# Kernel optimization log

Measured on AMD Instinct MI355X. Metric: run time of the kernel, lower is better.

## Reference

```python
import jax, jax.numpy as jnp
import numpy as np
from jax import lax

DILATIONS = (1, 2, 4)
K = 3        # kernel_size
HORIZON = 6


def _gcn(x, src, dst, W, b, n):
    # PyG GCNConv with self-loops: D^{-1/2}(A+I)D^{-1/2} X W + b
    xw = x @ W                                                # [N,H]
    e = src.shape[0]
    deg = 1.0 + jax.ops.segment_sum(jnp.ones((e,), x.dtype), dst, num_segments=n)
    dinv = lax.rsqrt(deg)                                     # [N]
    msg = xw[src] * (dinv[src] * dinv[dst])[:, None]          # [E,H]
    agg = jax.ops.segment_sum(msg, dst, num_segments=n)       # [N,H]
    return agg + xw * (dinv * dinv)[:, None] + b


def _cell(x, src, dst, win, gcn_w, gcn_b, conv_w, conv_b, proj_w, proj_b):
    n = x.shape[0]
    hg = jax.nn.relu(_gcn(x, src, dst, gcn_w, gcn_b, n))      # [N,H]
    tcn_in = jnp.concatenate([win[:, 1:], hg[:, None]], axis=1)  # [N,K,H]
    hin = jnp.transpose(tcn_in, (0, 2, 1))                    # [N,H,K]
    outs = []
    for i, d in enumerate(DILATIONS):
        p = (K - 1) * d // 2
        y = lax.conv_general_dilated(hin, conv_w[i], (1,), [(p, p)],
                                     rhs_dilation=(d,),
                                     dimension_numbers=('NCH', 'OIH', 'NCH'))
        outs.append(y[:, :, -1] + conv_b[i])                  # last temporal position, [N,H]
    h_new = jnp.concatenate(outs, axis=1) @ proj_w.T + proj_b  # [N,H]
    new_win = jnp.concatenate([win[:, 1:], h_new[:, None]], axis=1)
    return h_new, new_win


def reference(x_seq, edge_index_seq, edge_attr_seq, mask_seq, id_seq,
              gcn_w, gcn_b, conv_w, conv_b, proj_w, proj_b, head_w, head_b):
    T, N, _ = x_seq.shape
    H = gcn_w.shape[1]
    win0 = jnp.zeros((N, K, H), x_seq.dtype)

    def enc_step(win, inp):
        x_t, ei_t = inp
        _, win = _cell(x_t, ei_t[0], ei_t[1], win,
                       gcn_w, gcn_b, conv_w, conv_b, proj_w, proj_b)
        return win, None

    win, _ = lax.scan(enc_step, win0, (x_seq, edge_index_seq))

    src, dst = edge_index_seq[-1, 0], edge_index_seq[-1, 1]

    def dec_step(carry, _):
        win, inp = carry
        h_new, win = _cell(inp, src, dst, win,
                           gcn_w, gcn_b, conv_w, conv_b, proj_w, proj_b)
        y = h_new @ head_w.T + head_b                          # [N,C]
        return (win, y), y

    _, preds = lax.scan(dec_step, (win, x_seq[-1]), None, length=HORIZON)
    return preds  # [horizon, N, out_channels]


def setup_inputs() -> dict:
    T, N, F, E, H, C = 12, 20000, 16, 320000, 128, 16
    key = jax.random.key(0)
    ks = jax.random.split(key, 12)
    return {
        'x_seq': jax.random.normal(ks[0], (T, N, F), jnp.float32),
        'edge_index_seq': jax.random.randint(ks[1], (T, 2, E), 0, N, jnp.int64),
        'edge_attr_seq': jax.random.normal(ks[2], (T, E, 1), jnp.float32),
        'mask_seq': jnp.ones((T, N), jnp.bool_),
        'id_seq': jnp.tile(jnp.arange(N, dtype=jnp.int32)[None], (T, 1)),
        'gcn_w': jax.random.normal(ks[3], (F, H), jnp.float32) * 0.1,
        'gcn_b': jnp.zeros((H,), jnp.float32),
        'conv_w': jax.random.normal(ks[4], (3, H, H, K), jnp.float32) * 0.05,
        'conv_b': jnp.zeros((3, H), jnp.float32),
        'proj_w': jax.random.normal(ks[5], (H, 3 * H), jnp.float32) * 0.05,
        'proj_b': jnp.zeros((H,), jnp.float32),
        'head_w': jax.random.normal(ks[6], (C, H), jnp.float32) * 0.05,
        'head_b': jnp.zeros((C,), jnp.float32),
    }
```

## Files before the change

### kernel.cpp

```cpp
#include <hip/hip_runtime.h>

#define NN 20000
#define NP 20032
#define EE 320000
#define TT 12
#define HH 128
#define FF 16
#define CC 16
#define HOR 6

#define NB 313
#define WPT 84
#define CHE 3812

#define AGG_GRID 1896
#define HGA_GRID 15024

typedef __attribute__((ext_vector_type(8))) short short8;
typedef __attribute__((ext_vector_type(4))) float f32x4;

__device__ __forceinline__ float blo(unsigned int u) {
    union { float f; unsigned int i; } v; v.i = u << 16; return v.f;
}
__device__ __forceinline__ float bhi(unsigned int u) {
    union { float f; unsigned int i; } v; v.i = u & 0xffff0000u; return v.f;
}
__device__ __forceinline__ unsigned short f2b(float f) {
    union { float f; unsigned int i; } v; v.f = f;
    unsigned int x = v.i;
    return (unsigned short)((x + 0x7fffu + ((x >> 16) & 1u)) >> 16);
}
__device__ __forceinline__ unsigned int pck(float lo, float hi) {
    return ((unsigned int)f2b(hi) << 16) | f2b(lo);
}
__device__ __forceinline__ void addrow(float* acc, uint4 r) {
    acc[0] += blo(r.x); acc[1] += bhi(r.x);
    acc[2] += blo(r.y); acc[3] += bhi(r.y);
    acc[4] += blo(r.z); acc[5] += bhi(r.z);
    acc[6] += blo(r.w); acc[7] += bhi(r.w);
}

__global__ void k_zero(int* p, int n) {
    int i = blockIdx.x * 256 + threadIdx.x;
    if (i < n) p[i] = 0;
}

__global__ __launch_bounds__(512) void k_binA(const int* __restrict__ ei,
                                              int* __restrict__ gData,
                                              int* __restrict__ pcnt,
                                              int* __restrict__ pofs) {
    int wg = blockIdx.x;
    int t = wg / WPT, w = wg - t * WPT;
    __shared__ int lcnt[NB];
    __shared__ int sm[512];
    __shared__ __align__(16) int elist[CHE];
    int tid = threadIdx.x;
    for (int i = tid; i < NB; i += 512) lcnt[i] = 0;
    __syncthreads();
    int e0 = w * CHE, e1 = min(EE, e0 + CHE);
    int total = e1 - e0;
    const int* si = ei + (size_t)t * 2 * EE;
    const int* di = si + EE;
    int eA = e0 + tid * 4, eB = eA + 2048;
    bool hA = eA < e1, hB = eB < e1;
    int sA[4], dA[4], pA[4], sB[4], dB[4], pB[4];
    if (hA) {
        int4 s4 = *(const int4*)(si + eA);
        int4 d4 = *(const int4*)(di + eA);
        sA[0] = s4.x; sA[1] = s4.y; sA[2] = s4.z; sA[3] = s4.w;
        dA[0] = d4.x; dA[1] = d4.y; dA[2] = d4.z; dA[3] = d4.w;
    }
    if (hB) {
        int4 s4 = *(const int4*)(si + eB);
        int4 d4 = *(const int4*)(di + eB);
        sB[0] = s4.x; sB[1] = s4.y; sB[2] = s4.z; sB[3] = s4.w;
        dB[0] = d4.x; dB[1] = d4.y; dB[2] = d4.z; dB[3] = d4.w;
    }
    if (hA) {
#pragma unroll
        for (int k = 0; k < 4; k++) pA[k] = atomicAdd(&lcnt[dA[k] >> 6], 1);
    }
    if (hB) {
#pragma unroll
        for (int k = 0; k < 4; k++) pB[k] = atomicAdd(&lcnt[dB[k] >> 6], 1);
    }
    __syncthreads();
    sm[tid] = (tid < NB) ? lcnt[tid] : 0;
    __syncthreads();
    for (int off = 1; off < 512; off <<= 1) {
        int u = (tid >= off) ? sm[tid - off] : 0;
        __syncthreads();
        sm[tid] += u;
        __syncthreads();
    }
    if (tid < NB) {
        int v = lcnt[tid];
        int ex = sm[tid] - v;
        size_t o = (size_t)(t * WPT + w) * NB + tid;
        pcnt[o] = v;
        pofs[o] = ex;
        sm[tid] = ex;
    }
    __syncthreads();
    if (hA) {
#pragma unroll
        for (int k = 0; k < 4; k++) {
            int b = dA[k] >> 6;
            elist[sm[b] + pA[k]] = ((dA[k] & 63) << 16) | sA[k];
        }
    }
    if (hB) {
#pragma unroll
        for (int k = 0; k < 4; k++) {
            int b = dB[k] >> 6;
            elist[sm[b] + pB[k]] = ((dB[k] & 63) << 16) | sB[k];
        }
    }
    __syncthreads();
    int* gOut = gData + (size_t)(t * WPT + w) * CHE;
    for (int i = tid * 4; i < total; i += 2048)
        *(int4*)(gOut + i) = *(const int4*)&elist[i];
}

__global__ __launch_bounds__(512) void k_bscan2(const int* __restrict__ pcnt,
                                                int* __restrict__ bbase,
                                                int* __restrict__ rowptr) {
    int t = blockIdx.x, tid = threadIdx.x;
    __shared__ int sm[512];
    int v = 0;
    if (tid < NB)
        for (int w = 0; w < WPT; w++) v += pcnt[(size_t)(t * WPT + w) * NB + tid];
    sm[tid] = v;
    __syncthreads();
    for (int off = 1; off < 512; off <<= 1) {
        int u = (tid >= off) ? sm[tid - off] : 0;
        __syncthreads();
        sm[tid] += u;
        __syncthreads();
    }
    if (tid < NB) bbase[t * NB + tid] = sm[tid] - v;
    if (tid == 511) rowptr[(size_t)t * (NN + 1) + NN] = sm[511];
}

__global__ __launch_bounds__(256) void k_placeB(const int* __restrict__ gData,
                                                const int* __restrict__ pcnt,
                                                const int* __restrict__ pofs,
                                                const int* __restrict__ bbase,
                                                int* __restrict__ rowptr,
                                                float* __restrict__ dinv,
                                                unsigned short* __restrict__ csr) {
    int t = blockIdx.x / NB, b = blockIdx.x - t * NB;
    int tid = threadIdx.x;
    __shared__ int scnt[WPT], sofs[WPT], cofs[WPT + 1];
    __shared__ int elist[2048];
    __shared__ int cnt64[64], lofs[64], place[64];
    if (tid < WPT) {
        size_t o = (size_t)(t * WPT + tid) * NB + b;
        scnt[tid] = pcnt[o];
        sofs[tid] = pofs[o];
    }
    if (tid < 64) cnt64[tid] = 0;
    __syncthreads();
    if (tid == 0) {
        int s = 0;
        for (int w = 0; w < WPT; w++) { cofs[w] = s; s += scnt[w]; }
        cofs[WPT] = s;
    }
    __syncthreads();
    int total = cofs[WPT];
    int wv = tid >> 6, lane = tid & 63;
    for (int w = wv; w < WPT; w += 4) {
        int c = scnt[w], o = cofs[w];
        const int* sp = gData + (size_t)(t * WPT + w) * CHE + sofs[w];
        for (int i = lane; i < c; i += 64) elist[o + i] = sp[i];
    }
    __syncthreads();
    for (int i = tid; i < total; i += 256) atomicAdd(&cnt64[elist[i] >> 16], 1);
    __syncthreads();
    if (tid == 0) {
        int s = 0;
        for (int j = 0; j < 64; j++) { lofs[j] = s; place[j] = s; s += cnt64[j]; }
    }
    __syncthreads();
    int base = bbase[t * NB + b];
    int n = b * 64 + tid;
    if (tid < 64 && n < NN) {
        rowptr[(size_t)t * (NN + 1) + n] = base + lofs[tid];
        dinv[(size_t)t * NN + n] = rsqrtf(1.0f + (float)cnt64[tid]);
    }
    unsigned short* cbase = csr + (size_t)t * EE + base;
    for (int i = tid; i < total; i += 256) {
        int en = elist[i];
        int r = atomicAdd(&place[en >> 16], 1);
        cbase[r] = (unsigned short)(en & 0xffff);
    }
}

__global__ void k_count(const int* __restrict__ ei, int* __restrict__ cnt) {
    int idx = blockIdx.x * 256 + threadIdx.x;
    if (idx >= TT * EE) return;
    int t = idx / EE, e = idx - t * EE;
    int d = ei[t * 2 * EE + EE + e];
    atomicAdd(&cnt[t * NN + d], 1);
}

__global__ void k_dinvF(const int* __restrict__ cnt, float* __restrict__ dinv) {
    int idx = blockIdx.x * 256 + threadIdx.x;
    if (idx >= TT * NN) return;
    dinv[idx] = 1.0f / sqrtf(1.0f + (float)cnt[idx]);
}

__global__ void k_scan(const int* __restrict__ cnt, int* __restrict__ rowptr, int* __restrict__ wofs) {
    int t = blockIdx.x;
    const int* c = cnt + t * NN;
    int* rp = rowptr + t * (NN + 1);
    int* wo = wofs + t * NN;
    __shared__ int sums[1024];
    int tid = threadIdx.x;
    const int CH2 = 20;
    int base = tid * CH2;
    int loc[CH2];
    int s = 0;
    for (int i = 0; i < CH2; i++) { int ix = base + i; int v = (ix < NN) ? c[ix] : 0; loc[i] = s; s += v; }
    sums[tid] = s;
    __syncthreads();
    for (int off = 1; off < 1024; off <<= 1) {
        int v = (tid >= off) ? sums[tid - off] : 0;
        __syncthreads();
        sums[tid] += v;
        __syncthreads();
    }
    int excl = (tid > 0) ? sums[tid - 1] : 0;
    for (int i = 0; i < CH2; i++) {
        int ix = base + i;
        if (ix < NN) { int e = excl + loc[i]; rp[ix] = e; wo[ix] = e; }
    }
    if (tid == 1023) rp[NN] = sums[1023];
}

__global__ void k_place(const int* __restrict__ ei, int* __restrict__ wofs,
                        unsigned short* __restrict__ csr) {
    int idx = blockIdx.x * 256 + threadIdx.x;
    if (idx >= TT * EE) return;
    int t = idx / EE, e = idx - t * EE;
    int s = ei[t * 2 * EE + e];
    int d = ei[t * 2 * EE + EE + e];
    int pos = atomicAdd(&wofs[t * NN + d], 1);
    csr[t * EE + pos] = (unsigned short)s;
}

__global__ void k_wprepB(const float* __restrict__ cw, const float* __restrict__ pw,
                         const float* __restrict__ cb, const float* __restrict__ pb,
                         unsigned short* __restrict__ Bpk, float* __restrict__ Bf32,
                         float* __restrict__ bias) {
    int idx = blockIdx.x * 256 + threadIdx.x;
    if (blockIdx.x == 192) {
        int h = threadIdx.x;
        if (h < HH) {
            float m = pb[h];
            for (int d = 0; d < 3; d++)
                for (int o = 0; o < HH; o++)
                    m += cb[d * HH + o] * pw[h * 384 + d * HH + o];
            bias[h] = m;
        }
        return;
    }
    if (idx >= 384 * HH) return;
    int kk = idx / HH, h = idx - kk * HH;
    float m = 0.f;
    if (kk < 128) {
        int i = kk;
        for (int o = 0; o < HH; o++)
            m += cw[((1 * HH + o) * HH + i) * 3 + 0] * pw[h * 384 + 128 + o];
    } else if (kk < 256) {
        int i = kk - 128;
        for (int o = 0; o < HH; o++)
            m += cw[((0 * HH + o) * HH + i) * 3 + 0] * pw[h * 384 + o];
    } else {
        int i = kk - 256;
        for (int d = 0; d < 3; d++)
            for (int o = 0; o < HH; o++)
                m += cw[((d * HH + o) * HH + i) * 3 + 1] * pw[h * 384 + d * HH + o];
    }
    Bf32[kk * HH + h] = m;
    int ki = kk >> 5, r = kk & 31, q = r >> 3, j = r & 7, nt = h >> 4, ln = q * 16 + (h & 15);
    Bpk[(size_t)((ki * 8 + nt) * 64 + ln) * 8 + j] = f2b(m);
}

__global__ __launch_bounds__(128) void k_tchain(const float* __restrict__ Bf32,
                                                const float* __restrict__ biasT,
                                                unsigned short* __restrict__ Bq,
                                                float* __restrict__ biasQ) {
    __shared__ float v1[128], v2[128];
    int c = threadIdx.x;
    int r = blockIdx.x;
    const float* M2 = Bf32;
    const float* M1 = Bf32 + 128 * HH;
    const float* Mh = Bf32 + 256 * HH;
    if (r < 128) {
        int q4 = (r & 31) >> 3, jj = r & 7, rb = r >> 5;
        v1[c] = Mh[r * HH + c];
        v2[c] = 0.f;
        __syncthreads();
        {
            float val = v1[c];
            int kb0 = 10 * 4 + rb, nt0 = c >> 4, ln = q4 * 16 + (c & 15);
            Bq[((size_t)(kb0 * 16 + nt0) * 64 + ln) * 8 + jj] = f2b(val);
            int kb1 = 11 * 4 + rb, nt1 = 8 + (c >> 4);
            Bq[((size_t)(kb1 * 16 + nt1) * 64 + ln) * 8 + jj] = f2b(val);
        }
        for (int j = 1; j < 12; j++) {
            float acc = 0.f;
            for (int k = 0; k < 128; k++)
                acc += v1[k] * M1[k * HH + c] + v2[k] * M2[k * HH + c];
            __syncthreads();
            v2[c] = v1[c]; v1[c] = acc;
            __syncthreads();
            int ln = q4 * 16 + (c & 15);
            if (j <= 10) {
                int kb = (10 - j) * 4 + rb, nt = c >> 4;
                Bq[((size_t)(kb * 16 + nt) * 64 + ln) * 8 + jj] = f2b(acc);
            }
            {
                int kb = (11 - j) * 4 + rb, nt = 8 + (c >> 4);
                Bq[((size_t)(kb * 16 + nt) * 64 + ln) * 8 + jj] = f2b(acc);
            }
        }
        {
            int kb = 11 * 4 + rb, nt = c >> 4, ln = q4 * 16 + (c & 15);
            Bq[((size_t)(kb * 16 + nt) * 64 + ln) * 8 + jj] = 0;
        }
    } else {
        v1[c] = biasT[c];
        v2[c] = 0.f;
        __syncthreads();
        for (int j = 1; j < 12; j++) {
            float acc = biasT[c];
            for (int k = 0; k < 128; k++)
                acc += v1[k] * M1[k * HH + c] + v2[k] * M2[k * HH + c];
            __syncthreads();
            v2[c] = v1[c]; v1[c] = acc;
            __syncthreads();
        }
        biasQ[c] = v2[c];
        biasQ[128 + c] = v1[c];
    }
}

__global__ void k_xs(const float* __restrict__ x, const float* __restrict__ dinv,
                     unsigned short* __restrict__ xs) {
    int idx = blockIdx.x * 256 + threadIdx.x;
    if (idx >= TT * NN) return;
    float dn = dinv[idx];
    const float4* xr = (const float4*)(x + (size_t)idx * FF);
    unsigned int res[8];
#pragma unroll
    for (int k = 0; k < 4; k++) {
        float4 v = xr[k];
        res[2 * k]     = pck(v.x * dn, v.y * dn);
        res[2 * k + 1] = pck(v.z * dn, v.w * dn);
    }
    uint4* dst = (uint4*)(xs + (size_t)idx * FF);
    dst[0] = *(uint4*)(res);
    dst[1] = *(uint4*)(res + 4);
}

__global__ __launch_bounds__(256) void k_aggX(const unsigned short* __restrict__ xsA,
                                              const unsigned short* __restrict__ csrA,
                                              const int* __restrict__ rpA,
                                              const float* __restrict__ dinvA,
                                              float* __restrict__ zA) {
    int bid = blockIdx.x;
    int x = bid & 7, k = bid >> 3;
    int h = 3 * x + k / 79;
    int g = h >> 1;
    int nb = (h & 1) * 79 + (k % 79);
    int tid = threadIdx.x;
    int r = tid >> 1, eo = tid & 1;
    int n = nb * 128 + r;
    if (n >= NN) return;
    const unsigned short* xs = xsA + (size_t)g * NN * FF;
    const unsigned short* csr = csrA + (size_t)g * EE;
    const int* rp = rpA + (size_t)g * (NN + 1);
    float acc[16];
#pragma unroll
    for (int i = 0; i < 16; i++) acc[i] = 0.f;
    int j0 = rp[n], j1 = rp[n + 1];
    int j = j0 + eo;
    for (; j + 2 < j1; j += 4) {
        int s0 = csr[j], s1 = csr[j + 2];
        const uint4* p0 = (const uint4*)(xs + (size_t)s0 * FF);
        const uint4* p1 = (const uint4*)(xs + (size_t)s1 * FF);
        uint4 a0 = p0[0], a1 = p0[1], b0 = p1[0], b1 = p1[1];
        addrow(acc, a0); addrow(acc + 8, a1);
        addrow(acc, b0); addrow(acc + 8, b1);
    }
    if (j < j1) {
        const uint4* p0 = (const uint4*)(xs + (size_t)csr[j] * FF);
        uint4 a0 = p0[0], a1 = p0[1];
        addrow(acc, a0); addrow(acc + 8, a1);
    }
#pragma unroll
    for (int i = 0; i < 16; i++) acc[i] += __shfl_xor(acc[i], 1);
    if (eo == 0) {
        const uint4* sp = (const uint4*)(xs + (size_t)n * FF);
        uint4 a = sp[0], b4 = sp[1];
        addrow(acc, a); addrow(acc + 8, b4);
        float dn = dinvA[(size_t)g * NN + n];
        float4* zo = (float4*)(zA + (size_t)g * NP * FF + (size_t)n * FF);
#pragma unroll
        for (int k2 = 0; k2 < 4; k2++)
            zo[k2] = make_float4(acc[4 * k2] * dn, acc[4 * k2 + 1] * dn,
                                 acc[4 * k2 + 2] * dn, acc[4 * k2 + 3] * dn);
    }
}

__global__ __launch_bounds__(256) void k_hgA(const float* __restrict__ z12,
                                             const float* __restrict__ gw,
                                             const float* __restrict__ gb,
                                             unsigned short* __restrict__ hgAll) {
    int g = blockIdx.x * 256 + threadIdx.x;
    int row = g >> 4, cg = g & 15;
    int c0 = cg * 8;
    const float4* zp = (const float4*)(z12 + (size_t)row * FF);
    float4 z0 = zp[0], z1 = zp[1], z2 = zp[2], z3 = zp[3];
    float zr[16] = {z0.x, z0.y, z0.z, z0.w, z1.x, z1.y, z1.z, z1.w,
                    z2.x, z2.y, z2.z, z2.w, z3.x, z3.y, z3.z, z3.w};
    float s[8];
#pragma unroll
    for (int c = 0; c < 8; c++) s[c] = gb[c0 + c];
#pragma unroll
    for (int f = 0; f < 16; f++) {
        const float4* wp = (const float4*)(gw + f * HH + c0);
        float4 w0 = wp[0], w1 = wp[1];
        float zf = zr[f];
        s[0] += zf * w0.x; s[1] += zf * w0.y; s[2] += zf * w0.z; s[3] += zf * w0.w;
        s[4] += zf * w1.x; s[5] += zf * w1.y; s[6] += zf * w1.z; s[7] += zf * w1.w;
    }
    unsigned int res[4];
#pragma unroll
    for (int k = 0; k < 4; k++)
        res[k] = pck(fmaxf(s[2 * k], 0.f), fmaxf(s[2 * k + 1], 0.f));
    *(uint4*)(hgAll + (size_t)row * HH + c0) = *(uint4*)res;
}

__global__ __launch_bounds__(512, 4) void k_gemmE(const unsigned short* __restrict__ hgAll,
                                                  const unsigned short* __restrict__ Bq,
                                                  const float* __restrict__ biasQ,
                                                  unsigned short* __restrict__ out0,
                                                  unsigned short* __restrict__ out1) {
    __shared__ float bqs[256];
    __shared__ __align__(16) unsigned short csh[32 * 264];
    int tid = threadIdx.x;
    int wid = tid >> 6, lane = tid & 63;
    int rg = wid & 1, cg = wid >> 1;
    int m0b = blockIdx.x * 32;
    int m0 = m0b + rg * 16;
    int mr = lane & 15, q = lane >> 4;
    if (tid < 256) bqs[tid] = biasQ[tid];
    int nt0 = cg * 4;
    f32x4 acc[4];
#pragma unroll
    for (int j = 0; j < 4; j++) acc[j] = (f32x4){0.f, 0.f, 0.f, 0.f};
#pragma unroll
    for (int kb = 0; kb < 48; kb++) {
        short8 bf[4];
#pragma unroll
        for (int j = 0; j < 4; j++)
            bf[j] = *(const short8*)(Bq + ((size_t)(kb * 16 + nt0 + j) * 64 + lane) * 8);
        int s = kb >> 2;
        short8 af = *(const short8*)(hgAll + ((size_t)(s * NP) + m0 + mr) * HH +
                                     (kb & 3) * 32 + q * 8);
#pragma unroll
        for (int j = 0; j < 4; j++)
            acc[j] = __builtin_amdgcn_mfma_f32_16x16x32_bf16(af, bf[j], acc[j], 0, 0, 0);
    }
    __syncthreads();
#pragma unroll
    for (int j = 0; j < 4; j++) {
        int c = (nt0 + j) * 16 + mr;
        float bv = bqs[c];
#pragma unroll
        for (int r = 0; r < 4; r++)
            csh[(rg * 16 + q * 4 + r) * 264 + c] = f2b(acc[j][r] + bv);
    }
    __syncthreads();
#pragma unroll
    for (int i = 0; i < 2; i++) {
        int idx = i * 512 + tid;
        int row = idx >> 5, c8 = (idx & 31) * 8;
        short8 v = *(const short8*)&csh[row * 264 + c8];
        if (c8 < 128) *(short8*)(out0 + (size_t)(m0b + row) * HH + c8) = v;
        else          *(short8*)(out1 + (size_t)(m0b + row) * HH + (c8 - 128)) = v;
    }
}

__device__ __forceinline__ void hg_frag(const float* zsh, const float* Wg, const float* gbs,
                                        int mr, int q, short8* hgf) {
    float zr[16];
    {
        const float4* zp = (const float4*)(zsh + mr * FF);
        float4 z0 = zp[0], z1 = zp[1], z2 = zp[2], z3 = zp[3];
        zr[0] = z0.x; zr[1] = z0.y; zr[2] = z0.z; zr[3] = z0.w;
        zr[4] = z1.x; zr[5] = z1.y; zr[6] = z1.z; zr[7] = z1.w;
        zr[8] = z2.x; zr[9] = z2.y; zr[10] = z2.z; zr[11] = z2.w;
        zr[12] = z3.x; zr[13] = z3.y; zr[14] = z3.z; zr[15] = z3.w;
    }
#pragma unroll
    for (int k2 = 0; k2 < 4; k2++) {
        float s[8];
#pragma unroll
        for (int c = 0; c < 8; c++) s[c] = gbs[k2 * 32 + q * 8 + c];
#pragma unroll
        for (int f = 0; f < 16; f++) {
            const float4* wp = (const float4*)(Wg + f * HH + k2 * 32 + q * 8);
            float4 w0 = wp[0], w1 = wp[1];
            float zf = zr[f];
            s[0] += zf * w0.x; s[1] += zf * w0.y; s[2] += zf * w0.z; s[3] += zf * w0.w;
            s[4] += zf * w1.x; s[5] += zf * w1.y; s[6] += zf * w1.z; s[7] += zf * w1.w;
        }
#pragma unroll
        for (int c = 0; c < 8; c++) hgf[k2][c] = (short)f2b(fmaxf(s[c], 0.f));
    }
}

__global__ __launch_bounds__(256, 3) void k_gemmF2(const unsigned short* __restrict__ a0,
                                                   const unsigned short* __restrict__ a1,
                                                   const float* __restrict__ zt, int gather,
                                                   const float* __restrict__ gw,
                                                   const float* __restrict__ gb,
                                                   const unsigned short* __restrict__ Bpk,
                                                   const float* __restrict__ bias,
                                                   unsigned short* __restrict__ out,
                                                   const float* __restrict__ hw,
                                                   const float* __restrict__ hbv,
                                                   const float* __restrict__ dinvN,
                                                   const int* __restrict__ rp,
                                                   const unsigned short* __restrict__ csr,
                                                   unsigned short* __restrict__ xsD,
                                                   float* __restrict__ yout) {
    __shared__ float Wg[FF * HH];
    __shared__ float Whs[CC * 132];
    __shared__ float gbs[HH], biasS[HH], hbS[CC];
    __shared__ float zsh[16 * FF];
    __shared__ __align__(16) unsigned short hgD[16 * 136];
    __shared__ unsigned short hsh[16 * 136];
    __shared__ float ysh[16 * 17];
    int tid = threadIdx.x;
    int wid = tid >> 6, lane = tid & 63;
    int m0b = blockIdx.x * 16;
    int mr = lane & 15, q = lane >> 4;
    for (int i = tid; i < FF * HH; i += 256) {
        Wg[i] = gw[i];
        Whs[(i >> 7) * 132 + (i & 127)] = hw[i];
    }
    if (tid < HH) { gbs[tid] = gb[tid]; biasS[tid] = bias[tid]; }
    if (tid < CC) hbS[tid] = hbv[tid];
    if (!gather) {
        if (tid < 16 * FF) zsh[tid] = zt[(size_t)m0b * FF + tid];
    } else {
        int r = tid >> 4, p = tid & 15, half = p & 1, eo = p >> 1;
        int n = m0b + r;
        float a[8];
#pragma unroll
        for (int k = 0; k < 8; k++) a[k] = 0.f;
        if (n < NN) {
            int j0 = rp[n], j1 = rp[n + 1];
            for (int j = j0 + eo; j < j1; j += 8) {
                int s = csr[j];
                uint4 v = *(const uint4*)(xsD + (size_t)s * FF + half * 8);
                addrow(a, v);
            }
        }
#pragma unroll
        for (int k = 0; k < 8; k++) {
            a[k] += __shfl_xor(a[k], 2);
            a[k] += __shfl_xor(a[k], 4);
            a[k] += __shfl_xor(a[k], 8);
        }
        if (n < NN && eo == 0) {
            uint4 sv = *(const uint4*)(xsD + (size_t)n * FF + half * 8);
            addrow(a, sv);
            float dn = dinvN[n];
#pragma unroll
            for (int k = 0; k < 8; k++) zsh[r * FF + half * 8 + k] = a[k] * dn;
        }
    }
    __syncthreads();
    if (wid == 0) {
        short8 hgf[4];
        hg_frag(zsh, Wg, gbs, mr, q, hgf);
#pragma unroll
        for (int k2 = 0; k2 < 4; k2++)
            *(short8*)&hgD[mr * 136 + k2 * 32 + q * 8] = hgf[k2];
    }
    __syncthreads();
    int nt0 = wid * 2;
    f32x4 acc[2];
#pragma unroll
    for (int j = 0; j < 2; j++) acc[j] = (f32x4){0.f, 0.f, 0.f, 0.f};
#pragma unroll
    for (int ki = 0; ki < 12; ki++) {
        short8 bf[2];
#pragma unroll
        for (int j = 0; j < 2; j++)
            bf[j] = *(const short8*)(Bpk + (size_t)((ki * 8 + nt0 + j) * 64 + lane) * 8);
        short8 af;
        if (ki < 4)
            af = *(const short8*)(a0 + (size_t)(m0b + mr) * HH + ki * 32 + q * 8);
        else if (ki < 8)
            af = *(const short8*)(a1 + (size_t)(m0b + mr) * HH + (ki - 4) * 32 + q * 8);
        else
            af = *(const short8*)&hgD[mr * 136 + (ki - 8) * 32 + q * 8];
#pragma unroll
        for (int j = 0; j < 2; j++)
            acc[j] = __builtin_amdgcn_mfma_f32_16x16x32_bf16(af, bf[j], acc[j], 0, 0, 0);
    }
#pragma unroll
    for (int j = 0; j < 2; j++) {
        int feat = (nt0 + j) * 16 + mr;
        float bv = biasS[feat];
#pragma unroll
        for (int r = 0; r < 4; r++)
            hsh[(q * 4 + r) * 136 + feat] = f2b(acc[j][r] + bv);
    }
    __syncthreads();
    {
        int row = tid >> 4, c8 = (tid & 15) * 8;
        *(short8*)(out + (size_t)(m0b + row) * HH + c8) =
            *(const short8*)&hsh[row * 136 + c8];
    }
    {
        int r = tid >> 4, c = tid & 15;
        float y = hbS[c];
        for (int k = 0; k < HH; k++)
            y += blo((unsigned int)hsh[r * 136 + k]) * Whs[c * 132 + k];
        ysh[r * 17 + c] = y;
        int gn = m0b + r;
        if (gn < NN) yout[(size_t)gn * CC + c] = y;
    }
    __syncthreads();
    if (tid < 16) {
        int gn = m0b + tid;
        if (gn < NN) {
            float dn = dinvN[gn];
            unsigned int res[8];
#pragma unroll
            for (int k = 0; k < 8; k++)
                res[k] = pck(ysh[tid * 17 + 2 * k] * dn, ysh[tid * 17 + 2 * k + 1] * dn);
            uint4* dst = (uint4*)(xsD + (size_t)gn * FF);
            dst[0] = *(uint4*)(res);
            dst[1] = *(uint4*)(res + 4);
        }
    }
}

extern "C" void kernel_launch(void* const* d_in, const int* in_sizes, int n_in,
                              void* d_out, int out_size, void* d_ws, size_t ws_size,
                              hipStream_t stream) {
    const float* x_seq  = (const float*)d_in[0];
    const int*   ei     = (const int*)d_in[1];
    const float* gcn_w  = (const float*)d_in[5];
    const float* gcn_b  = (const float*)d_in[6];
    const float* conv_w = (const float*)d_in[7];
    const float* conv_b = (const float*)d_in[8];
    const float* proj_w = (const float*)d_in[9];
    const float* proj_b = (const float*)d_in[10];
    const float* head_w = (const float*)d_in[11];
    const float* head_b = (const float*)d_in[12];
    float* outp = (float*)d_out;

    char* ws = (char*)d_ws;
    size_t off = 0;
    auto alloc = [&](size_t bytes) { void* p = ws + off; off += (bytes + 255) & ~(size_t)255; return p; };
    float*          dinv   = (float*)alloc((size_t)TT * NN * 4);
    int*            rowptr = (int*)alloc((size_t)TT * (NN + 1) * 4);
    unsigned short* csr    = (unsigned short*)alloc((size_t)TT * EE * 2);
    unsigned short* hb0    = (unsigned short*)alloc((size_t)NP * HH * 2);
    unsigned short* hb1    = (unsigned short*)alloc((size_t)NP * HH * 2);
    unsigned short* hb2    = (unsigned short*)alloc((size_t)NP * HH * 2);
    unsigned short* hb3    = (unsigned short*)alloc((size_t)NP * HH * 2);
    unsigned short* xsD    = (unsigned short*)alloc((size_t)NP * FF * 2);
    unsigned short* Bpk    = (unsigned short*)alloc((size_t)384 * HH * 2);
    float*          Bf32   = (float*)alloc((size_t)384 * HH * 4);
    float*          biasT  = (float*)alloc(HH * 4);
    size_t tb = off;
    unsigned short* xs12  = (unsigned short*)alloc((size_t)TT * NN * FF * 2);
    float*          z12   = (float*)alloc((size_t)TT * NP * FF * 4);
    unsigned short* hgAll = (unsigned short*)alloc((size_t)TT * NP * HH * 2);
    unsigned short* Bq    = (unsigned short*)alloc((size_t)48 * 16 * 64 * 8 * 2);
    float*          biasQ = (float*)alloc(256 * 4);
    size_t compute_end = off;
    off = tb;
    int* gData = (int*)alloc((size_t)TT * WPT * CHE * 4);
    int* pcnt  = (int*)alloc((size_t)TT * WPT * NB * 4);
    int* pofs  = (int*)alloc((size_t)TT * WPT * NB * 4);
    int* bbase = (int*)alloc((size_t)TT * NB * 4);
    size_t csr_end = off;
    bool fastcsr = (csr_end <= ws_size && compute_end <= ws_size);

    if (fastcsr) {
        k_binA<<<TT * WPT, 512, 0, stream>>>(ei, gData, pcnt, pofs);
        k_bscan2<<<TT, 512, 0, stream>>>(pcnt, bbase, rowptr);
        k_placeB<<<TT * NB, 256, 0, stream>>>(gData, pcnt, pofs, bbase, rowptr, dinv, csr);
    } else {
        off = tb;
        int* cnt  = (int*)alloc((size_t)TT * NN * 4);
        int* wofs = (int*)alloc((size_t)TT * NN * 4);
        k_zero<<<(TT * NN + 255) / 256, 256, 0, stream>>>(cnt, TT * NN);
        k_count<<<(TT * EE + 255) / 256, 256, 0, stream>>>(ei, cnt);
        k_dinvF<<<(TT * NN + 255) / 256, 256, 0, stream>>>(cnt, dinv);
        k_scan<<<TT, 1024, 0, stream>>>(cnt, rowptr, wofs);
        k_place<<<(TT * EE + 255) / 256, 256, 0, stream>>>(ei, wofs, csr);
    }

    k_wprepB<<<193, 256, 0, stream>>>(conv_w, proj_w, conv_b, proj_b, Bpk, Bf32, biasT);
    k_tchain<<<129, 128, 0, stream>>>(Bf32, biasT, Bq, biasQ);

    k_xs<<<(TT * NN + 255) / 256, 256, 0, stream>>>(x_seq, dinv, xs12);
    k_aggX<<<AGG_GRID, 256, 0, stream>>>(xs12, csr, rowptr, dinv, z12);
    k_hgA<<<HGA_GRID, 256, 0, stream>>>(z12, gcn_w, gcn_b, hgAll);
    k_gemmE<<<NP / 32, 512, 0, stream>>>(hgAll, Bq, biasQ, hb2, hb3);

    unsigned short* hbuf[4] = {hb0, hb1, hb2, hb3};
    const float* dinv11 = dinv + (size_t)(TT - 1) * NN;
    const int* rp11 = rowptr + (size_t)(TT - 1) * (NN + 1);
    const unsigned short* csr11 = csr + (size_t)(TT - 1) * EE;
    for (int t = TT; t < TT + HOR; t++) {
        const float* zt = (t == TT) ? (z12 + (size_t)(TT - 1) * NP * FF) : nullptr;
        k_gemmF2<<<NP / 16, 256, 0, stream>>>(hbuf[(t + 2) & 3], hbuf[(t + 3) & 3],
                                              zt, (t == TT) ? 0 : 1,
                                              gcn_w, gcn_b, Bpk, biasT, hbuf[t & 3],
                                              head_w, head_b, dinv11, rp11, csr11,
                                              xsD, outp + (size_t)(t - TT) * NN * CC);
    }
}
```

Before: 498.8 us.

## Fuse GCN weight projection into encoder GEMM, dropping hgAll intermediate buffer

Removes the separate k_hgA kernel that wrote the full 12×N×128 bf16 hidden-state tensor to global memory. The GEMM kernel now computes relu(z·W+b) for its 32-row tile per timestep into shared memory, then feeds it to the MFMA loop. This cuts a large global write and re-read plus one launch. In exchange it adds per-step block syncs and serialises the small projection with the MFMA work, and the launch_bounds occupancy hint is dropped while shared memory use grows.

```diff
diff --git a/kernel.cpp b/kernel.cpp
--- a/kernel.cpp
+++ b/kernel.cpp
@@ -14,7 +14,6 @@
 #define CHE 3812
 
 #define AGG_GRID 1896
-#define HGA_GRID 15024
 
 typedef __attribute__((ext_vector_type(8))) short short8;
 typedef __attribute__((ext_vector_type(4))) float f32x4;
@@ -415,67 +414,70 @@
     }
 }
 
-__global__ __launch_bounds__(256) void k_hgA(const float* __restrict__ z12,
-                                             const float* __restrict__ gw,
-                                             const float* __restrict__ gb,
-                                             unsigned short* __restrict__ hgAll) {
-    int g = blockIdx.x * 256 + threadIdx.x;
-    int row = g >> 4, cg = g & 15;
-    int c0 = cg * 8;
-    const float4* zp = (const float4*)(z12 + (size_t)row * FF);
-    float4 z0 = zp[0], z1 = zp[1], z2 = zp[2], z3 = zp[3];
-    float zr[16] = {z0.x, z0.y, z0.z, z0.w, z1.x, z1.y, z1.z, z1.w,
-                    z2.x, z2.y, z2.z, z2.w, z3.x, z3.y, z3.z, z3.w};
-    float s[8];
-#pragma unroll
-    for (int c = 0; c < 8; c++) s[c] = gb[c0 + c];
-#pragma unroll
-    for (int f = 0; f < 16; f++) {
-        const float4* wp = (const float4*)(gw + f * HH + c0);
-        float4 w0 = wp[0], w1 = wp[1];
-        float zf = zr[f];
-        s[0] += zf * w0.x; s[1] += zf * w0.y; s[2] += zf * w0.z; s[3] += zf * w0.w;
-        s[4] += zf * w1.x; s[5] += zf * w1.y; s[6] += zf * w1.z; s[7] += zf * w1.w;
-    }
-    unsigned int res[4];
-#pragma unroll
-    for (int k = 0; k < 4; k++)
-        res[k] = pck(fmaxf(s[2 * k], 0.f), fmaxf(s[2 * k + 1], 0.f));
-    *(uint4*)(hgAll + (size_t)row * HH + c0) = *(uint4*)res;
-}
-
-__global__ __launch_bounds__(512, 4) void k_gemmE(const unsigned short* __restrict__ hgAll,
-                                                  const unsigned short* __restrict__ Bq,
-                                                  const float* __restrict__ biasQ,
-                                                  unsigned short* __restrict__ out0,
-                                                  unsigned short* __restrict__ out1) {
+__global__ __launch_bounds__(512) void k_gemmE(const float* __restrict__ z12,
+                                               const float* __restrict__ gw,
+                                               const float* __restrict__ gb,
+                                               const unsigned short* __restrict__ Bq,
+                                               const float* __restrict__ biasQ,
+                                               unsigned short* __restrict__ out0,
+                                               unsigned short* __restrict__ out1) {
+    __shared__ float Wg[FF * HH];
+    __shared__ float gbs[HH];
     __shared__ float bqs[256];
+    __shared__ __align__(16) unsigned short hgs[32 * 136];
     __shared__ __align__(16) unsigned short csh[32 * 264];
     int tid = threadIdx.x;
     int wid = tid >> 6, lane = tid & 63;
     int rg = wid & 1, cg = wid >> 1;
     int m0b = blockIdx.x * 32;
-    int m0 = m0b + rg * 16;
     int mr = lane & 15, q = lane >> 4;
-    if (tid < 256) bqs[tid] = biasQ[tid];
+    for (int i = tid; i < FF * HH; i += 512) Wg[i] = gw[i];
+    if (tid < HH) gbs[tid] = gb[tid];
+    if (tid >= 256 && tid < 512) bqs[tid - 256] = biasQ[tid - 256];
+    __syncthreads();
     int nt0 = cg * 4;
+    int hrow = tid >> 4, hc0 = (tid & 15) * 8;
     f32x4 acc[4];
 #pragma unroll
     for (int j = 0; j < 4; j++) acc[j] = (f32x4){0.f, 0.f, 0.f, 0.f};
-#pragma unroll
-    for (int kb = 0; kb < 48; kb++) {
-        short8 bf[4];
-#pragma unroll
-        for (int j = 0; j < 4; j++)
-            bf[j] = *(const short8*)(Bq + ((size_t)(kb * 16 + nt0 + j) * 64 + lane) * 8);
-        int s = kb >> 2;
-        short8 af = *(const short8*)(hgAll + ((size_t)(s * NP) + m0 + mr) * HH +
-                                     (kb & 3) * 32 + q * 8);
-#pragma unroll
-        for (int j = 0; j < 4; j++)
-            acc[j] = __builtin_amdgcn_mfma_f32_16x16x32_bf16(af, bf[j], acc[j], 0, 0, 0);
-    }
-    __syncthreads();
+    for (int s = 0; s < 12; s++) {
+        {
+            const float4* zp = (const float4*)(z12 + ((size_t)s * NP + m0b + hrow) * FF);
+            float4 z0 = zp[0], z1 = zp[1], z2 = zp[2], z3 = zp[3];
+            float zr[16] = {z0.x, z0.y, z0.z, z0.w, z1.x, z1.y, z1.z, z1.w,
+                            z2.x, z2.y, z2.z, z2.w, z3.x, z3.y, z3.z, z3.w};
+            float sv[8];
+#pragma unroll
+            for (int c = 0; c < 8; c++) sv[c] = gbs[hc0 + c];
+#pragma unroll
+            for (int f = 0; f < 16; f++) {
+                const float4* wp = (const float4*)(Wg + f * HH + hc0);
+                float4 w0 = wp[0], w1 = wp[1];
+                float zf = zr[f];
+                sv[0] += zf * w0.x; sv[1] += zf * w0.y; sv[2] += zf * w0.z; sv[3] += zf * w0.w;
+                sv[4] += zf * w1.x; sv[5] += zf * w1.y; sv[6] += zf * w1.z; sv[7] += zf * w1.w;
+            }
+            unsigned int res[4];
+#pragma unroll
+            for (int k = 0; k < 4; k++)
+                res[k] = pck(fmaxf(sv[2 * k], 0.f), fmaxf(sv[2 * k + 1], 0.f));
+            *(uint4*)&hgs[hrow * 136 + hc0] = *(uint4*)res;
+        }
+        __syncthreads();
+#pragma unroll
+        for (int k2 = 0; k2 < 4; k2++) {
+            int kb = s * 4 + k2;
+            short8 bf[4];
+#pragma unroll
+            for (int j = 0; j < 4; j++)
+                bf[j] = *(const short8*)(Bq + ((size_t)(kb * 16 + nt0 + j) * 64 + lane) * 8);
+            short8 af = *(const short8*)&hgs[(rg * 16 + mr) * 136 + k2 * 32 + q * 8];
+#pragma unroll
+            for (int j = 0; j < 4; j++)
+                acc[j] = __builtin_amdgcn_mfma_f32_16x16x32_bf16(af, bf[j], acc[j], 0, 0, 0);
+        }
+        __syncthreads();
+    }
 #pragma unroll
     for (int j = 0; j < 4; j++) {
         int c = (nt0 + j) * 16 + mr;
@@ -687,7 +689,6 @@
     size_t tb = off;
     unsigned short* xs12  = (unsigned short*)alloc((size_t)TT * NN * FF * 2);
     float*          z12   = (float*)alloc((size_t)TT * NP * FF * 4);
-    unsigned short* hgAll = (unsigned short*)alloc((size_t)TT * NP * HH * 2);
     unsigned short* Bq    = (unsigned short*)alloc((size_t)48 * 16 * 64 * 8 * 2);
     float*          biasQ = (float*)alloc(256 * 4);
     size_t compute_end = off;
@@ -719,8 +720,7 @@
 
     k_xs<<<(TT * NN + 255) / 256, 256, 0, stream>>>(x_seq, dinv, xs12);
     k_aggX<<<AGG_GRID, 256, 0, stream>>>(xs12, csr, rowptr, dinv, z12);
-    k_hgA<<<HGA_GRID, 256, 0, stream>>>(z12, gcn_w, gcn_b, hgAll);
-    k_gemmE<<<NP / 32, 512, 0, stream>>>(hgAll, Bq, biasQ, hb2, hb3);
+    k_gemmE<<<NP / 32, 512, 0, stream>>>(z12, gcn_w, gcn_b, Bq, biasQ, hb2, hb3);
 
     unsigned short* hbuf[4] = {hb0, hb1, hb2, hb3};
     const float* dinv11 = dinv + (size_t)(TT - 1) * NN;
```

Measured after the change: 439.1 us. -12.0%, faster.
